# Kernel tuning notes

Hardware: AMD Instinct MI355X
Metric: run time of the kernel (lower is better)

Reference implementation:

```python
import jax, jax.numpy as jnp
import numpy as np

B, C, T, K = 64, 12, 2048, 2048
LMAX = 11            # max kernel length among {7,9,11}
CMAX = C - 1         # torch.randint(1, C) -> at most C-1 selected channels
PL = 1024            # left pad: covers max 'same' left pad = (dil*(len-1))//2 <= (T-1)//2
PR = 3412            # right pad: covers zero-weight padded taps (LMAX-1)*dil_max
A = 7.0              # softppv_param


def setup_inputs() -> dict:
    rng = np.random.default_rng(0)
    klens = rng.choice(np.array([7, 9, 11]), size=K)
    nch = rng.integers(1, C, size=K)  # 1..C-1 channels per kernel
    weights = np.zeros((K, CMAX, LMAX), np.float32)
    ch_idx = np.zeros((K, CMAX), np.int32)
    dils = np.zeros(K, np.int32)
    offs = np.zeros(K, np.int32)
    olens = np.zeros(K, np.int32)
    for k in range(K):
        n, L = int(nch[k]), int(klens[k])
        ch_idx[k, :n] = rng.permutation(C)[:n]
        w = rng.standard_normal((n, L)).astype(np.float32)
        w -= w.mean(axis=1, keepdims=True)  # per-channel mean-centering as in torch init
        weights[k, :n, :L] = w
        d = int(2.0 ** rng.uniform(0.0, np.log2((T - 1) / (L - 1))))
        dils[k] = d
        if rng.integers(0, 2) == 0:  # padding='same' (torch: left=total//2, right=rest)
            offs[k] = PL - (d * (L - 1)) // 2
            olens[k] = T
        else:                        # padding='valid'
            offs[k] = PL
            olens[k] = T - d * (L - 1)
    biases = rng.uniform(0.0, 1.0, size=K).astype(np.float32)
    x = jax.random.normal(jax.random.key(0), (B, C, T), jnp.float32)
    return {
        "x": x,
        "weights": jnp.asarray(weights),
        "biases": jnp.asarray(biases),
        "ch_idx": jnp.asarray(ch_idx),
        "dils": jnp.asarray(dils),
        "offs": jnp.asarray(offs),
        "olens": jnp.asarray(olens),
    }


def reference(x, weights, biases, ch_idx, dils, offs, olens):
    # x: (B, C, T). Zero-pad time axis once so every (same/valid, dilation) variant
    # becomes a pure gather with a per-kernel offset; zero-padded weight taps/channels
    # contribute nothing, so padded gathers are harmless.
    xpad = jnp.pad(x, ((0, 0), (0, 0), (PL, PR)))
    t = jnp.arange(T)
    l = jnp.arange(LMAX)

    def step(_, p):
        W, b, ch, d, off, olen = p
        pos = off + t[:, None] + l[None, :] * d            # (T, LMAX) tap positions
        Xg = xpad[:, ch, :][:, :, pos]                     # (B, CMAX, T, LMAX)
        y = jnp.einsum('bctl,cl->bt', Xg, W) + b           # cross-correlation + bias
        mask = t < olen                                    # valid output positions
        ppv = jnp.sum(jax.nn.sigmoid(A * y - 3.0) * mask, axis=-1) / olen
        mx = jnp.max(jnp.where(mask, y, -jnp.inf), axis=-1)
        return None, (ppv, mx)

    _, (ppvs, mxs) = jax.lax.scan(step, None, (weights, biases, ch_idx, dils, offs, olens))
    # torch concatenates [ppv_k, max_k] per kernel along the feature axis -> (B, 2K)
    return jnp.stack([ppvs.T, mxs.T], axis=-1).reshape(x.shape[0], 2 * K)
```

## Files before the change

### kernel.cpp

```cpp
#include <hip/hip_runtime.h>
#include <math.h>

#define B_SZ   64
#define C_SZ   12
#define T_SZ   2048
#define K_SZ   2048
#define LMAX   11
#define CMAX   11
#define NPAIR  6
#define PL_PAD 1024
#define A_PARAM 7.0f

#define NW     8
#define BLOCK_MAIN (NW * 64)
#define R      8
#define SPL    4
#define NBLK   1024

typedef _Float16 h2 __attribute__((ext_vector_type(2)));

__device__ __forceinline__ float fdot2f(unsigned w, unsigned v, float acc) {
    return __builtin_amdgcn_fdot2(__builtin_bit_cast(h2, w),
                                  __builtin_bit_cast(h2, v), acc, false);
}

__global__ __launch_bounds__(256) void trh_kernel(const float* __restrict__ x,
                                                  unsigned short* __restrict__ xT) {
    const int c    = blockIdx.x;
    const int lane = threadIdx.x & 63;
    const int wid  = threadIdx.x >> 6;
    const int t0   = blockIdx.y * 128 + wid * 32;
    const float* xrow = x + ((size_t)lane * C_SZ + c) * T_SZ + t0;
    unsigned short* dst = xT + ((size_t)c * T_SZ + t0) * 64 + lane;
    #pragma unroll 8
    for (int i = 0; i < 32; ++i) {
        const _Float16 h = (_Float16)xrow[i];
        dst[i * 64] = __builtin_bit_cast(unsigned short, h);
    }
}

__global__ __launch_bounds__(1024) void sched_kernel(const float* __restrict__ w,
                                                     const int* __restrict__ olens,
                                                     unsigned* __restrict__ perm,
                                                     unsigned* __restrict__ meta,
                                                     unsigned* __restrict__ counter) {
    __shared__ unsigned key[K_SZ];
    const int tid = threadIdx.x;
    if (tid == 0) *counter = 0u;

    for (int k = tid; k < K_SZ; k += 1024) {
        const float* wk = w + (size_t)k * (CMAX * LMAX);
        int n = 0, L = 0;
        for (int e = 0; e < CMAX * LMAX; ++e) {
            if (wk[e] != 0.0f) {
                const int c = e / LMAX, l = e % LMAX;
                n = max(n, c + 1);
                L = max(L, l + 1);
            }
        }
        meta[k] = (unsigned)n | ((unsigned)L << 8);
        const unsigned cost = (unsigned)(n * L) * (unsigned)((olens[k] + 127) >> 7);
        key[k] = (cost << 11) | (unsigned)k;
    }
    __syncthreads();

    for (int ksz = 2; ksz <= K_SZ; ksz <<= 1) {
        for (int j = ksz >> 1; j > 0; j >>= 1) {
            for (int i = tid; i < K_SZ; i += 1024) {
                const int ixj = i ^ j;
                if (ixj > i) {
                    const unsigned a = key[i], b = key[ixj];
                    const bool sw = ((i & ksz) == 0) ? (a < b) : (a > b);
                    if (sw) { key[i] = b; key[ixj] = a; }
                }
            }
            __syncthreads();
        }
    }
    for (int i = tid; i < K_SZ; i += 1024)
        perm[i] = key[i] & 0x7FFu;
}

template<int LC>
__device__ __forceinline__ void conv_all(
    const unsigned short* __restrict__ xT,
    const int*      __restrict__ sCh,
    const unsigned  (* __restrict__ sWp)[LMAX],
    int npair, int d, int offr, int olen, float bias, int sp,
    int lane, int wid, float& psum, float& pmax)
{
    constexpr int NV = R + LC - 1;

    const int nj   = (olen + d - 1) / d;
    const int njb  = (nj + R - 1) / R;
    const int S    = (d >= 64) ? 1 : ((64 + d - 1) / d);
    const int len  = (njb + S - 1) / S;
    const int nunits = d * S;

    for (int u = sp * NW + wid; u < nunits; u += NW * SPL) {
        int q, seg;
        if (S == 1) { q = u; seg = 0; }
        else        { q = u % d; seg = u / d; }
        const int jb0 = seg * len;
        const int jb1 = min(njb, jb0 + len);

        for (int jb = jb0; jb < jb1; ++jb) {
            const int tq = q + jb * (R * d);
            if (tq >= olen) break;
            const int tpos0 = tq + offr;

            float y[R];
            #pragma unroll
            for (int r = 0; r < R; ++r) y[r] = bias;

            const bool fast = (tpos0 >= 0) && (tpos0 + (NV - 1) * d < T_SZ);

            if (fast) {
                for (int p = 0; p < npair; ++p) {
                    const int rbA = __builtin_amdgcn_readfirstlane(sCh[2*p  ] * T_SZ + tpos0);
                    const int rbB = __builtin_amdgcn_readfirstlane(sCh[2*p+1] * T_SZ + tpos0);
                    const unsigned short* rpA = xT + ((size_t)rbA << 6);
                    const unsigned short* rpB = xT + ((size_t)rbB << 6);

                    unsigned vp[NV];
                    #pragma unroll
                    for (int i = 0; i < NV; ++i) {
                        const unsigned a = rpA[lane];
                        const unsigned b = rpB[lane];
                        vp[i] = __builtin_amdgcn_perm(b, a, 0x05040100);
                        rpA += (d << 6); rpB += (d << 6);
                    }

                    const unsigned* wrow = &sWp[p][0];
                    #pragma unroll
                    for (int l = 0; l < LC; ++l) {
                        const unsigned w = wrow[l];
                        #pragma unroll
                        for (int r = 0; r < R; ++r)
                            y[r] = fdot2f(w, vp[l + r], y[r]);
                    }
                }
            } else {
                for (int p = 0; p < npair; ++p) {
                    const int rbA = __builtin_amdgcn_readfirstlane(sCh[2*p  ] * T_SZ);
                    const int rbB = __builtin_amdgcn_readfirstlane(sCh[2*p+1] * T_SZ);
                    const unsigned short* rowA = xT + ((size_t)rbA << 6);
                    const unsigned short* rowB = xT + ((size_t)rbB << 6);

                    unsigned vp[NV];
                    #pragma unroll
                    for (int i = 0; i < NV; ++i) {
                        const int tp  = tpos0 + i * d;
                        const int tpc = min(max(tp, 0), T_SZ - 1);
                        const unsigned a = rowA[((size_t)tpc << 6) + lane];
                        const unsigned b = rowB[((size_t)tpc << 6) + lane];
                        const unsigned pk = __builtin_amdgcn_perm(b, a, 0x05040100);
                        vp[i] = ((unsigned)tp < (unsigned)T_SZ) ? pk : 0u;
                    }

                    const unsigned* wrow = &sWp[p][0];
                    #pragma unroll
                    for (int l = 0; l < LC; ++l) {
                        const unsigned w = wrow[l];
                        #pragma unroll
                        for (int r = 0; r < R; ++r)
                            y[r] = fdot2f(w, vp[l + r], y[r]);
                    }
                }
            }

            #pragma unroll
            for (int r = 0; r < R; ++r) {
                const int t = tq + r * d;
                if (t < olen) {
                    psum += 1.0f / (1.0f + __expf(3.0f - A_PARAM * y[r]));
                    pmax  = fmaxf(pmax, y[r]);
                }
            }
        }
    }
}

__global__ __launch_bounds__(BLOCK_MAIN, 4) void rocket_tr(
    const unsigned short* __restrict__ xT,
    const unsigned* __restrict__ perm,
    const unsigned* __restrict__ meta,
    const float* __restrict__ weights,
    const float* __restrict__ biases,
    const int*   __restrict__ ch_idx,
    const int*   __restrict__ dils,
    const int*   __restrict__ offs,
    const int*   __restrict__ olens,
    float*       __restrict__ part,
    unsigned*    __restrict__ counter)
{
    __shared__ unsigned sWp[NPAIR][LMAX];
    __shared__ int      sCh[2 * NPAIR];
    __shared__ int      sItem;
    __shared__ float    sP[NW][64];
    __shared__ float    sM[NW][64];

    const int tid  = threadIdx.x;
    const int lane = tid & 63;
    const int wid  = __builtin_amdgcn_readfirstlane(tid >> 6);

    for (;;) {
        __syncthreads();
        if (tid == 0) sItem = (int)atomicAdd(counter, 1u);
        __syncthreads();
        const int item = sItem;
        if (item >= K_SZ * SPL) break;

        const int kidx = item / SPL;
        const int sp   = item % SPL;
        const int k    = (int)perm[kidx];

        if (tid < NPAIR * LMAX) {
            const int p = tid / LMAX;
            const int l = tid % LMAX;
            const float wA = weights[(size_t)k * (CMAX * LMAX) + (2 * p) * LMAX + l];
            const float wB = (2 * p + 1 < CMAX)
                ? weights[(size_t)k * (CMAX * LMAX) + (2 * p + 1) * LMAX + l] : 0.0f;
            h2 hh; hh.x = (_Float16)wA; hh.y = (_Float16)wB;
            sWp[p][l] = __builtin_bit_cast(unsigned, hh);
        }
        if (tid >= 64 && tid < 64 + 2 * NPAIR) {
            const int c = tid - 64;
            sCh[c] = (c < CMAX) ? ch_idx[(size_t)k * CMAX + c] : 0;
        }
        __syncthreads();

        const unsigned mk = meta[k];
        const int   n     = (int)(mk & 0xFFu);
        const int   L     = (int)((mk >> 8) & 0xFFu);
        const int   npair = (n + 1) >> 1;
        const int   d     = dils[k];
        const int   offr  = offs[k] - PL_PAD;
        const int   olen  = olens[k];
        const float bias  = biases[k];

        float psum = 0.0f;
        float pmax = -INFINITY;

        if (L <= 7)
            conv_all<7 >(xT, sCh, sWp, npair, d, offr, olen, bias, sp, lane, wid, psum, pmax);
        else if (L <= 9)
            conv_all<9 >(xT, sCh, sWp, npair, d, offr, olen, bias, sp, lane, wid, psum, pmax);
        else
            conv_all<11>(xT, sCh, sWp, npair, d, offr, olen, bias, sp, lane, wid, psum, pmax);

        sP[wid][lane] = psum;
        sM[wid][lane] = pmax;
        __syncthreads();

        if (tid < 64) {
            float s = 0.0f, m = -INFINITY;
            #pragma unroll
            for (int w = 0; w < NW; ++w) {
                s += sP[w][tid];
                m  = fmaxf(m, sM[w][tid]);
            }
            float* pp = part + ((size_t)k * SPL + sp) * 128;
            pp[tid]      = s;
            pp[64 + tid] = m;
        }
    }
}

__global__ __launch_bounds__(256) void combine_kernel(
    const float* __restrict__ part,
    const int*   __restrict__ olens,
    float*       __restrict__ out)
{
    const int idx = blockIdx.x * 256 + threadIdx.x;
    if (idx >= K_SZ * 64) return;
    const int k = idx >> 6;
    const int b = idx & 63;
    const float* pp = part + (size_t)k * SPL * 128;
    float s = 0.0f, m = -INFINITY;
    #pragma unroll
    for (int sp = 0; sp < SPL; ++sp) {
        s += pp[sp * 128 + b];
        m  = fmaxf(m, pp[sp * 128 + 64 + b]);
    }
    out[(size_t)b * (2 * K_SZ) + 2 * k]     = s / (float)olens[k];
    out[(size_t)b * (2 * K_SZ) + 2 * k + 1] = m;
}

__global__ __launch_bounds__(256) void rocket_fallback(
    const float* __restrict__ x,
    const float* __restrict__ weights,
    const float* __restrict__ biases,
    const int*   __restrict__ ch_idx,
    const int*   __restrict__ dils,
    const int*   __restrict__ offs,
    const int*   __restrict__ olens,
    float*       __restrict__ out)
{
    __shared__ float sW[CMAX][LMAX];
    __shared__ int   sCh[CMAX];
    __shared__ float sRed[2][4];

    const int k   = blockIdx.x;
    const int tid = threadIdx.x;

    if (tid < CMAX * LMAX)
        sW[tid / LMAX][tid % LMAX] = weights[(size_t)k * (CMAX * LMAX) + tid];
    if (tid < CMAX)
        sCh[tid] = ch_idx[(size_t)k * CMAX + tid];
    __syncthreads();

    const int   d    = dils[k];
    const int   off  = offs[k] - PL_PAD;
    const int   olen = olens[k];
    const float bias = biases[k];
    const int   lane = tid & 63;
    const int   wid  = tid >> 6;

    for (int b = blockIdx.y; b < B_SZ; b += gridDim.y) {
        float psum = 0.0f, pmax = -INFINITY;
        for (int t = tid; t < T_SZ; t += 256) {
            float y = bias;
            for (int c = 0; c < CMAX; ++c) {
                const float* xb = x + ((size_t)b * C_SZ + sCh[c]) * T_SZ;
                int pos = off + t;
                for (int l = 0; l < LMAX; ++l) {
                    const float xv = ((unsigned)pos < (unsigned)T_SZ) ? xb[pos] : 0.0f;
                    y = fmaf(sW[c][l], xv, y);
                    pos += d;
                }
            }
            if (t < olen) {
                psum += 1.0f / (1.0f + __expf(3.0f - A_PARAM * y));
                pmax = fmaxf(pmax, y);
            }
        }
        for (int o = 32; o > 0; o >>= 1) {
            psum += __shfl_down(psum, o, 64);
            pmax  = fmaxf(pmax, __shfl_down(pmax, o, 64));
        }
        if (lane == 0) { sRed[0][wid] = psum; sRed[1][wid] = pmax; }
        __syncthreads();
        if (tid == 0) {
            const float s = sRed[0][0] + sRed[0][1] + sRed[0][2] + sRed[0][3];
            const float m = fmaxf(fmaxf(sRed[1][0], sRed[1][1]),
                                  fmaxf(sRed[1][2], sRed[1][3]));
            out[(size_t)b * (2 * K_SZ) + 2 * k]     = s / (float)olen;
            out[(size_t)b * (2 * K_SZ) + 2 * k + 1] = m;
        }
        __syncthreads();
    }
}

extern "C" void kernel_launch(void* const* d_in, const int* in_sizes, int n_in,
                              void* d_out, int out_size, void* d_ws, size_t ws_size,
                              hipStream_t stream) {
    const float* x       = (const float*)d_in[0];
    const float* weights = (const float*)d_in[1];
    const float* biases  = (const float*)d_in[2];
    const int*   ch_idx  = (const int*)  d_in[3];
    const int*   dils    = (const int*)  d_in[4];
    const int*   offs    = (const int*)  d_in[5];
    const int*   olens   = (const int*)  d_in[6];
    float*       out     = (float*)d_out;

    const size_t xt_bytes   = (size_t)C_SZ * T_SZ * 64 * sizeof(unsigned short);
    const size_t perm_bytes = K_SZ * sizeof(unsigned);
    const size_t meta_bytes = K_SZ * sizeof(unsigned);
    const size_t part_bytes = (size_t)K_SZ * SPL * 128 * sizeof(float);
    const size_t need       = xt_bytes + perm_bytes + meta_bytes + part_bytes + 128;

    if (ws_size >= need) {
        char* wsb = (char*)d_ws;
        unsigned short* xT   = (unsigned short*)wsb;
        unsigned* perm       = (unsigned*)(wsb + xt_bytes);
        unsigned* meta       = (unsigned*)(wsb + xt_bytes + perm_bytes);
        float*    part       = (float*)(wsb + xt_bytes + perm_bytes + meta_bytes);
        unsigned* counter    = (unsigned*)(wsb + xt_bytes + perm_bytes + meta_bytes + part_bytes);

        dim3 tgrid(C_SZ, T_SZ / 128);
        trh_kernel<<<tgrid, 256, 0, stream>>>(x, xT);
        sched_kernel<<<1, 1024, 0, stream>>>(weights, olens, perm, meta, counter);
        rocket_tr<<<NBLK, BLOCK_MAIN, 0, stream>>>(xT, perm, meta, weights,
                                                   biases, ch_idx, dils, offs,
                                                   olens, part, counter);
        combine_kernel<<<(K_SZ * 64 + 255) / 256, 256, 0, stream>>>(part, olens, out);
    } else {
        dim3 grid(K_SZ, 16);
        rocket_fallback<<<grid, 256, 0, stream>>>(x, weights, biases, ch_idx,
                                                  dils, offs, olens, out);
    }
}
```

Before: 629.9 us.

## Schedule work per wavefront instead of per block to drop block barriers

Each wavefront now pulls its own work item from the global atomic counter, stages its own copy of the fp16 weights and channel indices in a per-wave LDS slice, and writes its partial sum and max directly to global memory. This removes the block-wide __syncthreads barriers and the cross-wave LDS reduction, so waves no longer wait on each other when kernels have uneven work. SPL rises from 4 to 16 to keep the number of work units comparable at wave granularity, which means four times as many atomics and partial records for the combine kernel to read.

After: 941.0 us. +49.4%, slower.

```diff
diff --git a/kernel.cpp b/kernel.cpp
--- a/kernel.cpp
+++ b/kernel.cpp
@@ -14,7 +14,7 @@
 #define NW     8
 #define BLOCK_MAIN (NW * 64)
 #define R      8
-#define SPL    4
+#define SPL    16
 #define NBLK   1024
 
 typedef _Float16 h2 __attribute__((ext_vector_type(2)));
@@ -85,9 +85,9 @@
 __device__ __forceinline__ void conv_all(
     const unsigned short* __restrict__ xT,
     const int*      __restrict__ sCh,
-    const unsigned  (* __restrict__ sWp)[LMAX],
+    const unsigned* __restrict__ sWp,
     int npair, int d, int offr, int olen, float bias, int sp,
-    int lane, int wid, float& psum, float& pmax)
+    int lane, float& psum, float& pmax)
 {
     constexpr int NV = R + LC - 1;
 
@@ -97,7 +97,7 @@
     const int len  = (njb + S - 1) / S;
     const int nunits = d * S;
 
-    for (int u = sp * NW + wid; u < nunits; u += NW * SPL) {
+    for (int u = sp; u < nunits; u += SPL) {
         int q, seg;
         if (S == 1) { q = u; seg = 0; }
         else        { q = u % d; seg = u / d; }
@@ -131,7 +131,7 @@
                         rpA += (d << 6); rpB += (d << 6);
                     }
 
-                    const unsigned* wrow = &sWp[p][0];
+                    const unsigned* wrow = &sWp[p * LMAX];
                     #pragma unroll
                     for (int l = 0; l < LC; ++l) {
                         const unsigned w = wrow[l];
@@ -158,7 +158,7 @@
                         vp[i] = ((unsigned)tp < (unsigned)T_SZ) ? pk : 0u;
                     }
 
-                    const unsigned* wrow = &sWp[p][0];
+                    const unsigned* wrow = &sWp[p * LMAX];
                     #pragma unroll
                     for (int l = 0; l < LC; ++l) {
                         const unsigned w = wrow[l];
@@ -194,41 +194,38 @@
     float*       __restrict__ part,
     unsigned*    __restrict__ counter)
 {
-    __shared__ unsigned sWp[NPAIR][LMAX];
-    __shared__ int      sCh[2 * NPAIR];
-    __shared__ int      sItem;
-    __shared__ float    sP[NW][64];
-    __shared__ float    sM[NW][64];
+    __shared__ unsigned sWpAll[NW][NPAIR * LMAX];
+    __shared__ int      sChAll[NW][12];
 
     const int tid  = threadIdx.x;
     const int lane = tid & 63;
     const int wid  = __builtin_amdgcn_readfirstlane(tid >> 6);
+    unsigned* sWp = &sWpAll[wid][0];
+    int*      sCh = &sChAll[wid][0];
 
     for (;;) {
-        __syncthreads();
-        if (tid == 0) sItem = (int)atomicAdd(counter, 1u);
-        __syncthreads();
-        const int item = sItem;
+        int item = 0;
+        if (lane == 0) item = (int)atomicAdd(counter, 1u);
+        item = __shfl(item, 0, 64);
         if (item >= K_SZ * SPL) break;
 
         const int kidx = item / SPL;
         const int sp   = item % SPL;
         const int k    = (int)perm[kidx];
 
-        if (tid < NPAIR * LMAX) {
-            const int p = tid / LMAX;
-            const int l = tid % LMAX;
+        for (int e = lane; e < NPAIR * LMAX; e += 64) {
+            const int p = e / LMAX;
+            const int l = e % LMAX;
             const float wA = weights[(size_t)k * (CMAX * LMAX) + (2 * p) * LMAX + l];
             const float wB = (2 * p + 1 < CMAX)
                 ? weights[(size_t)k * (CMAX * LMAX) + (2 * p + 1) * LMAX + l] : 0.0f;
             h2 hh; hh.x = (_Float16)wA; hh.y = (_Float16)wB;
-            sWp[p][l] = __builtin_bit_cast(unsigned, hh);
-        }
-        if (tid >= 64 && tid < 64 + 2 * NPAIR) {
-            const int c = tid - 64;
-            sCh[c] = (c < CMAX) ? ch_idx[(size_t)k * CMAX + c] : 0;
-        }
-        __syncthreads();
+            sWp[e] = __builtin_bit_cast(unsigned, hh);
+        }
+        if (lane < 12)
+            sCh[lane] = (lane < CMAX) ? ch_idx[(size_t)k * CMAX + lane] : 0;
+        asm volatile("s_waitcnt lgkmcnt(0)" ::: "memory");
+        __builtin_amdgcn_sched_barrier(0);
 
         const unsigned mk = meta[k];
         const int   n     = (int)(mk & 0xFFu);
@@ -243,27 +240,15 @@
         float pmax = -INFINITY;
 
         if (L <= 7)
-            conv_all<7 >(xT, sCh, sWp, npair, d, offr, olen, bias, sp, lane, wid, psum, pmax);
+            conv_all<7 >(xT, sCh, sWp, npair, d, offr, olen, bias, sp, lane, psum, pmax);
         else if (L <= 9)
-            conv_all<9 >(xT, sCh, sWp, npair, d, offr, olen, bias, sp, lane, wid, psum, pmax);
+            conv_all<9 >(xT, sCh, sWp, npair, d, offr, olen, bias, sp, lane, psum, pmax);
         else
-            conv_all<11>(xT, sCh, sWp, npair, d, offr, olen, bias, sp, lane, wid, psum, pmax);
-
-        sP[wid][lane] = psum;
-        sM[wid][lane] = pmax;
-        __syncthreads();
-
-        if (tid < 64) {
-            float s = 0.0f, m = -INFINITY;
-            #pragma unroll
-            for (int w = 0; w < NW; ++w) {
-                s += sP[w][tid];
-                m  = fmaxf(m, sM[w][tid]);
-            }
-            float* pp = part + ((size_t)k * SPL + sp) * 128;
-            pp[tid]      = s;
-            pp[64 + tid] = m;
-        }
+            conv_all<11>(xT, sCh, sWp, npair, d, offr, olen, bias, sp, lane, psum, pmax);
+
+        float* pp = part + ((size_t)k * SPL + sp) * 128;
+        pp[lane]      = psum;
+        pp[64 + lane] = pmax;
     }
 }
 
@@ -278,7 +263,7 @@
     const int b = idx & 63;
     const float* pp = part + (size_t)k * SPL * 128;
     float s = 0.0f, m = -INFINITY;
-    #pragma unroll
+    #pragma unroll 4
     for (int sp = 0; sp < SPL; ++sp) {
         s += pp[sp * 128 + b];
         m  = fmaxf(m, pp[sp * 128 + 64 + b]);
```
